# Performance work log

Measured on AMD Instinct MI355X. Metric: run time of the kernel, lower is better.

## Reference

```python
import jax, jax.numpy as jnp
import numpy as np
import math

N, D, BITS = 2048, 1024, 8
K = 1 << BITS          # 256 centroids
NG = (D + 1) // 2      # 512 rotation groups

def setup_inputs() -> dict:
    key = jax.random.key(0)
    kx, kc, kr = jax.random.split(key, 3)
    x = jax.random.normal(kx, (N, D), dtype=jnp.float32)
    # Lloyd-Max style scalar codebook: sorted centroids for a Gaussian source
    centroids = jnp.sort(jax.random.normal(kc, (K,), dtype=jnp.float32))
    # random planar rotations: [cos(theta), sin(theta)] per 2D group
    angles = jax.random.uniform(kr, (NG,), dtype=jnp.float32) * (2.0 * math.pi)
    rot2 = jnp.stack([jnp.cos(angles), jnp.sin(angles)], axis=-1)  # [NG, 2]
    return {"x": x, "centroids": centroids, "rot2": rot2}

def reference(x, centroids, rot2):
    d = x.shape[-1]
    n_groups = rot2.shape[0]
    d_padded = 2 * n_groups
    # unit-normalize rows
    norms = jnp.clip(jnp.linalg.norm(x, axis=-1, keepdims=True), 1e-8)  # [N,1]
    x_unit = x / norms
    pad = d_padded - d
    if pad > 0:
        x_unit = jnp.pad(x_unit, [(0, 0)] * (x.ndim - 1) + [(0, pad)])
    v = x_unit.reshape(*x.shape[:-1], n_groups, 2)                      # [N,NG,2]
    c, s = rot2[..., 0], rot2[..., 1]
    v0, v1 = v[..., 0], v[..., 1]
    v_rot = jnp.stack([c * v0 - s * v1, s * v0 + c * v1], axis=-1)      # rotate
    flat = v_rot.reshape(*v_rot.shape[:-2], -1)                         # [N,d_padded]
    # per-scalar nearest-centroid quantization
    indices = jnp.argmin(jnp.abs(flat[..., None] - centroids), axis=-1) # [N,d_padded]
    values = centroids[indices]
    v_q = values.reshape(*values.shape[:-1], n_groups, 2)
    q0, q1 = v_q[..., 0], v_q[..., 1]
    v_rec = jnp.stack([c * q0 + s * q1, -s * q0 + c * q1], axis=-1)     # inverse rotate
    x_hat = v_rec.reshape(*v_rec.shape[:-2], -1)[..., :d] * norms       # rescale
    return (x_hat, indices)
```

## Files before the change

### kernel.cpp

```cpp
#include <hip/hip_runtime.h>
#include <cfloat>

#define NROWS 2048
#define DDIM  1024
#define KCEN  256
#define NBINS 2048

__global__ __launch_bounds__(256)
void planar_quant_kernel(const float* __restrict__ x,
                         const float* __restrict__ cen,
                         const float* __restrict__ rot,
                         float* __restrict__ out_xhat,
                         float* __restrict__ out_idx)
{
    __shared__ float s_cen[KCEN];
    __shared__ float s_mid[KCEN];
    __shared__ unsigned short s_base[NBINS];
    __shared__ float s_red[4];
    __shared__ float s_norm;

    const int row = blockIdx.x;
    const int t   = threadIdx.x;

    const float4 xv = *(const float4*)(x + (size_t)row * DDIM + 4 * t);
    const float4 rv = *(const float4*)(rot + 4 * t);
    const float  cv = cen[t];

    s_cen[t] = cv;

    float ss = xv.x * xv.x + xv.y * xv.y + xv.z * xv.z + xv.w * xv.w;
    #pragma unroll
    for (int off = 32; off >= 1; off >>= 1)
        ss += __shfl_xor(ss, off, 64);
    if ((t & 63) == 0) s_red[t >> 6] = ss;

    __syncthreads();

    if (t == 0) {
        const float tot = s_red[0] + s_red[1] + s_red[2] + s_red[3];
        s_norm = fmaxf(sqrtf(tot), 1e-8f);
    }

    const float lo    = 0.5f * (s_cen[0] + s_cen[1]);
    const float hi    = 0.5f * (s_cen[KCEN - 2] + s_cen[KCEN - 1]);
    const float invw  = (float)NBINS / fmaxf(hi - lo, 1e-30f);
    const float nbm1f = (float)(NBINS - 1);

#define BIN_OF(m) ((int)fminf(fmaxf(((m) - (lo)) * invw, 0.0f), nbm1f))

    {
        const float cm    = s_cen[(t > 0) ? (t - 1) : 0];
        const float cp    = s_cen[(t < KCEN - 1) ? (t + 1) : (KCEN - 1)];
        const float mid_c = (t < KCEN - 1) ? 0.5f * (cv + cp) : FLT_MAX;
        s_mid[t] = mid_c;

        const int jc = BIN_OF(mid_c);
        const int jp = (t > 0) ? BIN_OF(0.5f * (cm + cv)) : -1;
        for (int b = jp + 1; b <= jc; ++b)
            s_base[b] = (unsigned short)t;
    }

    __syncthreads();

    const float nrm = s_norm;
    const float inv = 1.0f / nrm;

    const float v0 = xv.x * inv, v1 = xv.y * inv, v2 = xv.z * inv, v3 = xv.w * inv;

    const float r0 = rv.x * v0 - rv.y * v1;
    const float r1 = rv.y * v0 + rv.x * v1;
    const float r2 = rv.z * v2 - rv.w * v3;
    const float r3 = rv.w * v2 + rv.z * v3;

    int i0 = s_base[BIN_OF(r0)];
    int i1 = s_base[BIN_OF(r1)];
    int i2 = s_base[BIN_OF(r2)];
    int i3 = s_base[BIN_OF(r3)];

    while (true) {
        const float m0 = s_mid[i0], m1 = s_mid[i1], m2 = s_mid[i2], m3 = s_mid[i3];
        const int c0 = m0 < r0, c1 = m1 < r1, c2 = m2 < r2, c3 = m3 < r3;
        if (!__any(c0 | c1 | c2 | c3)) break;
        i0 += c0; i1 += c1; i2 += c2; i3 += c3;
    }

    const int   ii[4] = {i0, i1, i2, i3};
    const float rr[4] = {r0, r1, r2, r3};
    int   qi[4];
    float qv[4];
    #pragma unroll
    for (int e = 0; e < 4; ++e) {
        const int   idx = ii[e];
        const float v   = rr[e];
        const int   im  = (idx > 0) ? idx - 1 : 0;
        const int   ip  = (idx < KCEN - 1) ? idx + 1 : KCEN - 1;
        const float cc  = s_cen[idx];
        const float cl  = s_cen[im];
        const float cr  = s_cen[ip];
        const float best = fabsf(v - cc);
        if (idx > 0 && fabsf(v - cl) <= best)            { qi[e] = im;  qv[e] = cl; }
        else if (idx < KCEN - 1 && fabsf(v - cr) < best) { qi[e] = ip;  qv[e] = cr; }
        else                                             { qi[e] = idx; qv[e] = cc; }
    }

    float4 xh;
    xh.x = ( rv.x * qv[0] + rv.y * qv[1]) * nrm;
    xh.y = (-rv.y * qv[0] + rv.x * qv[1]) * nrm;
    xh.z = ( rv.z * qv[2] + rv.w * qv[3]) * nrm;
    xh.w = (-rv.w * qv[2] + rv.z * qv[3]) * nrm;

    float4 fi;
    fi.x = (float)qi[0]; fi.y = (float)qi[1]; fi.z = (float)qi[2]; fi.w = (float)qi[3];

    const size_t off = (size_t)row * DDIM + 4 * t;
    *(float4*)(out_xhat + off) = xh;
    *(float4*)(out_idx  + off) = fi;
#undef BIN_OF
}

extern "C" void kernel_launch(void* const* d_in, const int* in_sizes, int n_in,
                              void* d_out, int out_size, void* d_ws, size_t ws_size,
                              hipStream_t stream) {
    const float* x   = (const float*)d_in[0];
    const float* cen = (const float*)d_in[1];
    const float* rot = (const float*)d_in[2];
    float* out       = (float*)d_out;

    planar_quant_kernel<<<NROWS, 256, 0, stream>>>(
        x, cen, rot, out, out + (size_t)NROWS * DDIM);
}
```

Before: 71.39 us.

## Process one row per wavefront to amortize codebook table setup across four rows

Each 256-thread block now handles four rows, one per wave, with each lane holding 16 elements. The row norm is reduced with wave shuffles only, so the shared-memory reduction and its extra barrier are gone. The centroid, midpoint and bin tables are built once per four rows, which cuts the per-row setup cost and the block count by four. In exchange the grid shrinks to 512 blocks, register pressure rises, and the wave-wide search loop runs until the slowest of 16 elements per lane has converged.

```diff
diff --git a/kernel.cpp b/kernel.cpp
--- a/kernel.cpp
+++ b/kernel.cpp
@@ -5,6 +5,7 @@
 #define DDIM  1024
 #define KCEN  256
 #define NBINS 2048
+#define RPB   4
 
 __global__ __launch_bounds__(256)
 void planar_quant_kernel(const float* __restrict__ x,
@@ -16,105 +17,110 @@
     __shared__ float s_cen[KCEN];
     __shared__ float s_mid[KCEN];
     __shared__ unsigned short s_base[NBINS];
-    __shared__ float s_red[4];
-    __shared__ float s_norm;
 
-    const int row = blockIdx.x;
-    const int t   = threadIdx.x;
+    const int t    = threadIdx.x;
+    const int lane = t & 63;
+    const int wave = t >> 6;
+    const int row  = blockIdx.x * RPB + wave;
+    const size_t rbase = (size_t)row * DDIM;
 
-    const float4 xv = *(const float4*)(x + (size_t)row * DDIM + 4 * t);
-    const float4 rv = *(const float4*)(rot + 4 * t);
-    const float  cv = cen[t];
+    float4 xv[4], rv[4];
+    #pragma unroll
+    for (int c = 0; c < 4; ++c) {
+        const int off = 256 * c + 4 * lane;
+        xv[c] = *(const float4*)(x   + rbase + off);
+        rv[c] = *(const float4*)(rot + off);
+    }
 
+    const float cv = cen[t];
+    const float cm = (t > 0)        ? cen[t - 1] : cv;
+    const float cp = (t < KCEN - 1) ? cen[t + 1] : cv;
     s_cen[t] = cv;
 
-    float ss = xv.x * xv.x + xv.y * xv.y + xv.z * xv.z + xv.w * xv.w;
-    #pragma unroll
-    for (int off = 32; off >= 1; off >>= 1)
-        ss += __shfl_xor(ss, off, 64);
-    if ((t & 63) == 0) s_red[t >> 6] = ss;
-
-    __syncthreads();
-
-    if (t == 0) {
-        const float tot = s_red[0] + s_red[1] + s_red[2] + s_red[3];
-        s_norm = fmaxf(sqrtf(tot), 1e-8f);
-    }
-
-    const float lo    = 0.5f * (s_cen[0] + s_cen[1]);
-    const float hi    = 0.5f * (s_cen[KCEN - 2] + s_cen[KCEN - 1]);
+    const float lo    = 0.5f * (cen[0] + cen[1]);
+    const float hi    = 0.5f * (cen[KCEN - 2] + cen[KCEN - 1]);
     const float invw  = (float)NBINS / fmaxf(hi - lo, 1e-30f);
     const float nbm1f = (float)(NBINS - 1);
+#define BIN_OF(m) ((int)fminf(fmaxf(((m) - lo) * invw, 0.0f), nbm1f))
 
-#define BIN_OF(m) ((int)fminf(fmaxf(((m) - (lo)) * invw, 0.0f), nbm1f))
-
+    const float mid_c = (t < KCEN - 1) ? 0.5f * (cv + cp) : FLT_MAX;
+    s_mid[t] = mid_c;
     {
-        const float cm    = s_cen[(t > 0) ? (t - 1) : 0];
-        const float cp    = s_cen[(t < KCEN - 1) ? (t + 1) : (KCEN - 1)];
-        const float mid_c = (t < KCEN - 1) ? 0.5f * (cv + cp) : FLT_MAX;
-        s_mid[t] = mid_c;
-
         const int jc = BIN_OF(mid_c);
         const int jp = (t > 0) ? BIN_OF(0.5f * (cm + cv)) : -1;
         for (int b = jp + 1; b <= jc; ++b)
             s_base[b] = (unsigned short)t;
     }
 
+    float ss = 0.f;
+    #pragma unroll
+    for (int c = 0; c < 4; ++c)
+        ss += xv[c].x * xv[c].x + xv[c].y * xv[c].y
+            + xv[c].z * xv[c].z + xv[c].w * xv[c].w;
+    #pragma unroll
+    for (int off = 32; off >= 1; off >>= 1)
+        ss += __shfl_xor(ss, off, 64);
+    const float nrm = fmaxf(sqrtf(ss), 1e-8f);
+    const float inv = 1.0f / nrm;
+
     __syncthreads();
 
-    const float nrm = s_norm;
-    const float inv = 1.0f / nrm;
+    float r[16];
+    #pragma unroll
+    for (int c = 0; c < 4; ++c) {
+        const float v0 = xv[c].x * inv, v1 = xv[c].y * inv;
+        const float v2 = xv[c].z * inv, v3 = xv[c].w * inv;
+        r[4*c + 0] = rv[c].x * v0 - rv[c].y * v1;
+        r[4*c + 1] = rv[c].y * v0 + rv[c].x * v1;
+        r[4*c + 2] = rv[c].z * v2 - rv[c].w * v3;
+        r[4*c + 3] = rv[c].w * v2 + rv[c].z * v3;
+    }
 
-    const float v0 = xv.x * inv, v1 = xv.y * inv, v2 = xv.z * inv, v3 = xv.w * inv;
-
-    const float r0 = rv.x * v0 - rv.y * v1;
-    const float r1 = rv.y * v0 + rv.x * v1;
-    const float r2 = rv.z * v2 - rv.w * v3;
-    const float r3 = rv.w * v2 + rv.z * v3;
-
-    int i0 = s_base[BIN_OF(r0)];
-    int i1 = s_base[BIN_OF(r1)];
-    int i2 = s_base[BIN_OF(r2)];
-    int i3 = s_base[BIN_OF(r3)];
+    int idx[16];
+    #pragma unroll
+    for (int e = 0; e < 16; ++e)
+        idx[e] = s_base[BIN_OF(r[e])];
 
     while (true) {
-        const float m0 = s_mid[i0], m1 = s_mid[i1], m2 = s_mid[i2], m3 = s_mid[i3];
-        const int c0 = m0 < r0, c1 = m1 < r1, c2 = m2 < r2, c3 = m3 < r3;
-        if (!__any(c0 | c1 | c2 | c3)) break;
-        i0 += c0; i1 += c1; i2 += c2; i3 += c3;
+        int any = 0;
+        #pragma unroll
+        for (int e = 0; e < 16; ++e) {
+            const int c = s_mid[idx[e]] < r[e];
+            any |= c;
+            idx[e] += c;
+        }
+        if (!__any(any)) break;
     }
 
-    const int   ii[4] = {i0, i1, i2, i3};
-    const float rr[4] = {r0, r1, r2, r3};
-    int   qi[4];
-    float qv[4];
+    float qv[16];
     #pragma unroll
-    for (int e = 0; e < 4; ++e) {
-        const int   idx = ii[e];
-        const float v   = rr[e];
-        const int   im  = (idx > 0) ? idx - 1 : 0;
-        const int   ip  = (idx < KCEN - 1) ? idx + 1 : KCEN - 1;
-        const float cc  = s_cen[idx];
-        const float cl  = s_cen[im];
-        const float cr  = s_cen[ip];
+    for (int e = 0; e < 16; ++e) {
+        const int   i  = idx[e];
+        const float v  = r[e];
+        const int   im = (i > 0) ? i - 1 : 0;
+        const int   ip = (i < KCEN - 1) ? i + 1 : KCEN - 1;
+        const float cc = s_cen[i];
+        const float cl = s_cen[im];
+        const float cr = s_cen[ip];
         const float best = fabsf(v - cc);
-        if (idx > 0 && fabsf(v - cl) <= best)            { qi[e] = im;  qv[e] = cl; }
-        else if (idx < KCEN - 1 && fabsf(v - cr) < best) { qi[e] = ip;  qv[e] = cr; }
-        else                                             { qi[e] = idx; qv[e] = cc; }
+        if (i > 0 && fabsf(v - cl) <= best)            { idx[e] = im; qv[e] = cl; }
+        else if (i < KCEN - 1 && fabsf(v - cr) < best) { idx[e] = ip; qv[e] = cr; }
+        else                                           { qv[e] = cc; }
     }
 
-    float4 xh;
-    xh.x = ( rv.x * qv[0] + rv.y * qv[1]) * nrm;
-    xh.y = (-rv.y * qv[0] + rv.x * qv[1]) * nrm;
-    xh.z = ( rv.z * qv[2] + rv.w * qv[3]) * nrm;
-    xh.w = (-rv.w * qv[2] + rv.z * qv[3]) * nrm;
-
-    float4 fi;
-    fi.x = (float)qi[0]; fi.y = (float)qi[1]; fi.z = (float)qi[2]; fi.w = (float)qi[3];
-
-    const size_t off = (size_t)row * DDIM + 4 * t;
-    *(float4*)(out_xhat + off) = xh;
-    *(float4*)(out_idx  + off) = fi;
+    #pragma unroll
+    for (int c = 0; c < 4; ++c) {
+        float4 xh, fi;
+        xh.x = ( rv[c].x * qv[4*c + 0] + rv[c].y * qv[4*c + 1]) * nrm;
+        xh.y = (-rv[c].y * qv[4*c + 0] + rv[c].x * qv[4*c + 1]) * nrm;
+        xh.z = ( rv[c].z * qv[4*c + 2] + rv[c].w * qv[4*c + 3]) * nrm;
+        xh.w = (-rv[c].w * qv[4*c + 2] + rv[c].z * qv[4*c + 3]) * nrm;
+        fi.x = (float)idx[4*c + 0]; fi.y = (float)idx[4*c + 1];
+        fi.z = (float)idx[4*c + 2]; fi.w = (float)idx[4*c + 3];
+        const size_t off = rbase + 256 * c + 4 * lane;
+        *(float4*)(out_xhat + off) = xh;
+        *(float4*)(out_idx  + off) = fi;
+    }
 #undef BIN_OF
 }
 
@@ -126,6 +132,6 @@
     const float* rot = (const float*)d_in[2];
     float* out       = (float*)d_out;
 
-    planar_quant_kernel<<<NROWS, 256, 0, stream>>>(
+    planar_quant_kernel<<<NROWS / RPB, 256, 0, stream>>>(
         x, cen, rot, out, out + (size_t)NROWS * DDIM);
 }
```

After: 71.19 us. About the same (-0.3%).
